# Kernel optimization log

Hardware: AMD Instinct MI355X
Metric: run time of the kernel (lower is better)

## Reference

```python
import jax, jax.numpy as jnp
import numpy as np

CPJ = 8
HID = 256
PARENTS = [-1,0,0,0,1,2,3,4,5,6,7,8,9,9,9,12,13,14,16,17,18,19]
SPARSE_IDX = list(range(54))

def _extend(nodes, cpj, parents=None):
    nodes = list(nodes)
    if parents is not None:
        while nodes[-1] != 0:
            nodes.append(parents[nodes[-1]])
    return [j * cpj + k for j in nodes for k in range(cpj)]

DQ_IN = _extend([0,3,6,9,12,13,14,15,16,17,18,19,20,21], CPJ, PARENTS)  # 21 nodes -> 168 ch
OUT1 = _extend([9], CPJ)          # 8 ch
OUT2 = _extend([6, 9, 12], CPJ)   # 24 ch
OUT3 = _extend([0, 3, 6], CPJ)    # 24 ch
IN_DIM = len(DQ_IN) + len(SPARSE_IDX)  # 222


def _mlp_params(key, out_dim):
    k = jax.random.split(key, 6)
    s = lambda fan_in: 1.0 / np.sqrt(fan_in)
    return (
        jax.random.uniform(k[0], (IN_DIM, HID), jnp.float32, -s(IN_DIM), s(IN_DIM)),
        jax.random.uniform(k[1], (HID,), jnp.float32, -s(IN_DIM), s(IN_DIM)),
        jax.random.uniform(k[2], (HID, HID), jnp.float32, -s(HID), s(HID)),
        jax.random.uniform(k[3], (HID,), jnp.float32, -s(HID), s(HID)),
        jax.random.uniform(k[4], (HID, out_dim), jnp.float32, -s(HID), s(HID)),
        jax.random.uniform(k[5], (out_dim,), jnp.float32, -s(HID), s(HID)),
    )


def setup_inputs() -> dict:
    key = jax.random.key(0)
    ks = jax.random.split(key, 5)
    B, T = 1024, 128
    inp = {
        'sparse_input': jax.random.normal(ks[0], (B, T, 54), jnp.float32),
        'decoder_output': jax.random.normal(ks[1], (B, T, 22 * CPJ), jnp.float32),
    }
    for i, (k, od) in enumerate(zip(ks[2:5], (len(OUT1), len(OUT2), len(OUT3))), start=1):
        p = _mlp_params(k, od)
        for j, name in enumerate(('w0', 'b0', 'w1', 'b1', 'w2', 'b2')):
            inp[f'{name}_{i}'] = p[j]
    return inp


def _mlp(x, w0, b0, w1, b1, w2, b2):
    h = jax.nn.leaky_relu(x @ w0 + b0, 0.01)
    h = jax.nn.leaky_relu(h @ w1 + b1, 0.01)
    return h @ w2 + b2


def reference(sparse_input, decoder_output,
              w0_1, b0_1, w1_1, b1_1, w2_1, b2_1,
              w0_2, b0_2, w1_2, b1_2, w2_2, b2_2,
              w0_3, b0_3, w1_3, b1_3, w2_3, b2_3):
    sp = sparse_input[:, :, jnp.array(SPARSE_IDX)]
    d = decoder_output
    # pass 1
    x = jnp.concatenate((d[:, :, jnp.array(DQ_IN)], sp), axis=2)
    res1 = _mlp(x, w0_1, b0_1, w1_1, b1_1, w2_1, b2_1)
    d = d.at[:, :, jnp.array(OUT1)].set(res1)
    # pass 2
    x = jnp.concatenate((d[:, :, jnp.array(DQ_IN)], sp), axis=2)
    res2 = _mlp(x, w0_2, b0_2, w1_2, b1_2, w2_2, b2_2)
    d = d.at[:, :, jnp.array(OUT2)].set(res2)
    # pass 3
    x = jnp.concatenate((d[:, :, jnp.array(DQ_IN)], sp), axis=2)
    res3 = _mlp(x, w0_3, b0_3, w1_3, b1_3, w2_3, b2_3)
    return res3
```

## Files before the change

kernel.cpp:

```cpp
#include <hip/hip_runtime.h>

typedef __bf16 bf16x8 __attribute__((ext_vector_type(8)));
typedef __bf16 bf16x4 __attribute__((ext_vector_type(4)));
typedef float  f32x16 __attribute__((ext_vector_type(16)));

#define DDEC  176
#define DSP   54
#define HID   256
#define RPW   32
#define WPB   4
#define BM    (RPW * WPB)
#define CSZ   8192
#define W1_OFF 65536
#define W2_OFF 131072
#define MLP_WS 139264

struct Biases { const float* b1[3]; const float* b2[3]; };

__global__ __launch_bounds__(256) void prep_weights(
    const float* __restrict__ w0a, const float* __restrict__ w1a, const float* __restrict__ w2a,
    const float* __restrict__ w0b, const float* __restrict__ w1b, const float* __restrict__ w2b,
    const float* __restrict__ w0c, const float* __restrict__ w1c, const float* __restrict__ w2c,
    const float* __restrict__ b0a, const float* __restrict__ b0b, const float* __restrict__ b0c,
    __bf16* __restrict__ ws)
{
  int idx = blockIdx.x * 256 + threadIdx.x;
  if (idx >= 3 * MLP_WS) return;
  int m = idx / MLP_WS;
  int r = idx - m * MLP_WS;
  const float* w0 = (m == 0) ? w0a : (m == 1) ? w0b : w0c;
  const float* w1 = (m == 0) ? w1a : (m == 1) ? w1b : w1c;
  const float* w2 = (m == 0) ? w2a : (m == 1) ? w2b : w2c;
  const float* b0 = (m == 0) ? b0a : (m == 1) ? b0b : b0c;
  float v;
  if (r < W1_OFF) {
    int n = r >> 8, k = r & 255;
    v = (k < 222) ? w0[k * HID + n] : (k == 222 ? b0[n] : 0.0f);
  } else if (r < W2_OFF) {
    int rr = r - W1_OFF;
    int n = rr >> 8, k = rr & 255;
    v = w1[k * HID + n];
  } else {
    int rr = r - W2_OFF;
    int n = rr >> 8, k = rr & 255;
    int od = (m == 0) ? 8 : 24;
    v = (n < od) ? w2[k * od + n] : 0.0f;
  }
  ws[idx] = (__bf16)v;
}

__device__ __forceinline__ float lrelu(float v) { return v > 0.f ? v : 0.01f * v; }

__device__ __forceinline__ void gload16(const void* g, void* l) {
  __builtin_amdgcn_global_load_lds(
      (const __attribute__((address_space(1))) void*)g,
      (__attribute__((address_space(3))) void*)l, 16, 0, 0);
}

__device__ __forceinline__ void stage(const __bf16* __restrict__ wsrc, __bf16* buf, int tid) {
  #pragma unroll
  for (int r = 0; r < 4; ++r) {
    const int a  = (r * 256 + tid) * 16;
    const int lc = a >> 9;
    const int un = (a & 511) ^ ((lc & 31) << 4);
    gload16(wsrc + lc * 256 + (un >> 1), (char*)buf + r * 4096 + (tid >> 6) * 1024);
  }
}

template<int NKK>
__device__ __forceinline__ void gemm1(const __bf16* buf, const bf16x8* bfr,
                                      f32x16& acc, int r32, int h) {
  const int sw = r32 << 4;
  const char* abase = (const char*)buf + (r32 << 9);
  #pragma unroll
  for (int kk = 0; kk < NKK; ++kk) {
    const int inner = ((kk << 5) + (h << 4)) ^ sw;
    bf16x8 a0 = *(const bf16x8*)(abase + inner);
    acc = __builtin_amdgcn_mfma_f32_32x32x16_bf16(a0, bfr[kk], acc, 0, 0, 0);
  }
}

__device__ __forceinline__ bf16x4 shfl32(bf16x4 x) {
  union { bf16x4 v; unsigned long long u; } t;
  t.v = x;
  t.u = __shfl_xor(t.u, 32, 64);
  return t.v;
}
__device__ __forceinline__ bf16x8 cat44(bf16x4 lo, bf16x4 hi) {
  return (bf16x8){lo[0], lo[1], lo[2], lo[3], hi[0], hi[1], hi[2], hi[3]};
}

struct Frag2 { bf16x8 f0, f1; };

template<bool BIAS, bool LR>
__device__ __forceinline__ Frag2 d2frags(const f32x16 acc, const float* bias, int h) {
  bf16x4 pk[4];
  #pragma unroll
  for (int t = 0; t < 4; ++t) {
    float bx = 0.f, by = 0.f, bz = 0.f, bw = 0.f;
    if (BIAS) {
      float4 bv = *(const float4*)(bias + 8 * t + 4 * h);
      bx = bv.x; by = bv.y; bz = bv.z; bw = bv.w;
    }
    float v0 = acc[4 * t] + bx, v1 = acc[4 * t + 1] + by;
    float v2 = acc[4 * t + 2] + bz, v3 = acc[4 * t + 3] + bw;
    if (LR) { v0 = lrelu(v0); v1 = lrelu(v1); v2 = lrelu(v2); v3 = lrelu(v3); }
    pk[t] = (bf16x4){(__bf16)v0, (__bf16)v1, (__bf16)v2, (__bf16)v3};
  }
  bf16x4 r1 = shfl32(h ? pk[0] : pk[1]);
  bf16x4 r2 = shfl32(h ? pk[2] : pk[3]);
  Frag2 out;
  out.f0 = h ? cat44(r1, pk[1]) : cat44(pk[0], r1);
  out.f1 = h ? cat44(r2, pk[3]) : cat44(pk[2], r2);
  return out;
}

__device__ __forceinline__ bf16x8 packf44(float4 a, float4 b) {
  return (bf16x8){(__bf16)a.x, (__bf16)a.y, (__bf16)a.z, (__bf16)a.w,
                  (__bf16)b.x, (__bf16)b.y, (__bf16)b.z, (__bf16)b.w};
}
__device__ __forceinline__ bf16x8 packf2222(float2 a, float2 b, float2 c, float2 d) {
  return (bf16x8){(__bf16)a.x, (__bf16)a.y, (__bf16)b.x, (__bf16)b.y,
                  (__bf16)c.x, (__bf16)c.y, (__bf16)d.x, (__bf16)d.y};
}

__global__ __launch_bounds__(256, 2) void trunk_fused(
    const float* __restrict__ sparse, const float* __restrict__ dec,
    const __bf16* __restrict__ ws, float* __restrict__ out, Biases bp)
{
  __shared__ __align__(16) __bf16 lds[16384];
  __bf16* const buf0 = lds;
  __bf16* const buf1 = lds + CSZ;

  const int tid  = threadIdx.x;
  const int lane = tid & 63;
  const int wid  = tid >> 6;
  const int r32  = lane & 31;
  const int h    = lane >> 5;
  const long grow = (long)blockIdx.x * BM + wid * RPW + r32;

  stage(ws, buf0, tid);

  bf16x8 xb[14];
  {
    constexpr int ND[21] = {0,3,6,9,12,13,14,15,16,17,18,19,20,21,19,17,14,9,6,3,0};
    const float* drow = dec + grow * DDEC;
    const float* srow = sparse + grow * DSP;
    #pragma unroll
    for (int kf = 0; kf < 14; ++kf) {
      if (kf <= 9) {
        const int off = (h ? ND[2 * kf + 1] : ND[2 * kf]) * 8;
        const float4* p = (const float4*)(drow + off);
        xb[kf] = packf44(p[0], p[1]);
      } else if (kf == 10) {
        if (h == 0) {
          const float4* p = (const float4*)(drow + ND[20] * 8);
          xb[kf] = packf44(p[0], p[1]);
        } else {
          const float2* q = (const float2*)(srow + 0);
          xb[kf] = packf2222(q[0], q[1], q[2], q[3]);
        }
      } else if (kf <= 12) {
        const float2* q = (const float2*)(srow + (2 * kf + h - 21) * 8);
        xb[kf] = packf2222(q[0], q[1], q[2], q[3]);
      } else {
        if (h == 0) {
          const float2* q = (const float2*)(srow + 40);
          xb[kf] = packf2222(q[0], q[1], q[2], q[3]);
        } else {
          const float2* q = (const float2*)(srow + 48);
          xb[kf] = packf2222(q[0], q[1], q[2], make_float2(1.0f, 0.0f));
        }
      }
    }
  }
  __syncthreads();
  int pb = 0;

  for (int m = 0; m < 3; ++m) {
    const __bf16* W0 = ws + m * MLP_WS;
    const __bf16* W1 = W0 + W1_OFF;
    const __bf16* W2 = W0 + W2_OFF;
    const float* b1 = bp.b1[m];
    const float* b2 = bp.b2[m];

    bf16x8 hb1[16];
    f32x16 a2 = {};

    #pragma unroll
    for (int c = 0; c < 8; ++c) {
      __bf16* cur = pb ? buf1 : buf0;
      __bf16* nxt = pb ? buf0 : buf1;
      stage(c < 7 ? W0 + (c + 1) * CSZ : W1, nxt, tid);
      f32x16 acc = {};
      gemm1<14>(cur, xb, acc, r32, h);
      Frag2 t = d2frags<false, true>(acc, nullptr, h);
      hb1[2 * c]     = t.f0;
      hb1[2 * c + 1] = t.f1;
      __syncthreads();
      pb ^= 1;
    }

    #pragma unroll
    for (int c = 0; c < 8; ++c) {
      __bf16* cur = pb ? buf1 : buf0;
      __bf16* nxt = pb ? buf0 : buf1;
      const __bf16* w2f = W2 + r32 * 256 + h * 8 + 32 * c;
      bf16x8 wa0 = *(const bf16x8*)(w2f + 0);
      bf16x8 wa1 = *(const bf16x8*)(w2f + 16);
      if (c < 7)      stage(W1 + (c + 1) * CSZ, nxt, tid);
      else if (m < 2) stage(ws + (m + 1) * MLP_WS, nxt, tid);
      f32x16 acc = {};
      gemm1<16>(cur, hb1, acc, r32, h);
      Frag2 t = d2frags<true, true>(acc, b1 + 32 * c, h);
      a2 = __builtin_amdgcn_mfma_f32_32x32x16_bf16(wa0, t.f0, a2, 0, 0, 0);
      a2 = __builtin_amdgcn_mfma_f32_32x32x16_bf16(wa1, t.f1, a2, 0, 0, 0);
      __syncthreads();
      pb ^= 1;
    }

    if (m == 2) {
      #pragma unroll
      for (int t = 0; t < 3; ++t) {
        const int c0 = 8 * t + 4 * h;
        float4 bv = *(const float4*)(b2 + c0);
        float4 o;
        o.x = a2[4 * t]     + bv.x;
        o.y = a2[4 * t + 1] + bv.y;
        o.z = a2[4 * t + 2] + bv.z;
        o.w = a2[4 * t + 3] + bv.w;
        *(float4*)(out + grow * 24 + c0) = o;
      }
    } else {
      bf16x4 pk[3];
      #pragma unroll
      for (int t = 0; t < 3; ++t) {
        const int c0 = 8 * t + 4 * h;
        float4 bv = *(const float4*)(b2 + c0);
        pk[t] = (bf16x4){(__bf16)(a2[4 * t] + bv.x),     (__bf16)(a2[4 * t + 1] + bv.y),
                         (__bf16)(a2[4 * t + 2] + bv.z), (__bf16)(a2[4 * t + 3] + bv.w)};
      }
      if (m == 0) {
        bf16x4 r = shfl32(pk[0]);
        if (h) { bf16x8 f = cat44(r, pk[0]); xb[1] = f; xb[8] = f; }
      } else {
        bf16x4 r1 = shfl32(h ? pk[0] : pk[1]);
        bf16x4 r2 = shfl32(pk[2]);
        if (h) {
          bf16x8 fJ9 = cat44(r1, pk[1]);  xb[1] = fJ9;  xb[8] = fJ9;
        } else {
          bf16x8 fJ6  = cat44(pk[0], r1); xb[1] = fJ6;  xb[9] = fJ6;
          bf16x8 fJ12 = cat44(pk[2], r2); xb[2] = fJ12;
        }
      }
    }
  }
}

extern "C" void kernel_launch(void* const* d_in, const int* in_sizes, int n_in,
                              void* d_out, int out_size, void* d_ws, size_t ws_size,
                              hipStream_t stream)
{
  const float* sparse = (const float*)d_in[0];
  const float* dec    = (const float*)d_in[1];
  Biases bp;
  const float* w0[3]; const float* w1[3]; const float* w2[3]; const float* b0[3];
  for (int m = 0; m < 3; ++m) {
    w0[m]    = (const float*)d_in[2 + m * 6 + 0];
    b0[m]    = (const float*)d_in[2 + m * 6 + 1];
    w1[m]    = (const float*)d_in[2 + m * 6 + 2];
    bp.b1[m] = (const float*)d_in[2 + m * 6 + 3];
    w2[m]    = (const float*)d_in[2 + m * 6 + 4];
    bp.b2[m] = (const float*)d_in[2 + m * 6 + 5];
  }
  __bf16* ws = (__bf16*)d_ws;
  const int nrows = in_sizes[0] / DSP;

  const int prep_total = 3 * MLP_WS;
  prep_weights<<<(prep_total + 255) / 256, 256, 0, stream>>>(
      w0[0], w1[0], w2[0], w0[1], w1[1], w2[1], w0[2], w1[2], w2[2],
      b0[0], b0[1], b0[2], ws);

  const int nblocks = nrows / BM;
  trunk_fused<<<nblocks, 256, 0, stream>>>(sparse, dec, ws, (float*)d_out, bp);
}
```

Baseline: 136.6 us.

## Stage weight chunks in pairs with split accumulators and LDS-cached biases

Doubles the weight staging chunk so each pipeline step covers 64 hidden columns. That halves the number of barrier and stage rounds per MLP and lets two independent MFMA chains run per k-step, and the first layer also splits accumulators by even and odd k to break the dependency chain. Biases are copied into LDS once, and s_setprio is raised around the MFMA sections. The cost is double the LDS per block (64KB for weights plus the bias area), which can cut occupancy below the 2-blocks-per-CU launch bound, and more accumulator registers.

```diff
diff --git a/kernel.cpp b/kernel.cpp
--- a/kernel.cpp
+++ b/kernel.cpp
@@ -11,6 +11,7 @@
 #define WPB   4
 #define BM    (RPW * WPB)
 #define CSZ   8192
+#define PSZ   16384
 #define W1_OFF 65536
 #define W2_OFF 131072
 #define MLP_WS 139264
@@ -57,9 +58,9 @@
       (__attribute__((address_space(3))) void*)l, 16, 0, 0);
 }
 
-__device__ __forceinline__ void stage(const __bf16* __restrict__ wsrc, __bf16* buf, int tid) {
+__device__ __forceinline__ void stage2(const __bf16* __restrict__ wsrc, __bf16* buf, int tid) {
   #pragma unroll
-  for (int r = 0; r < 4; ++r) {
+  for (int r = 0; r < 8; ++r) {
     const int a  = (r * 256 + tid) * 16;
     const int lc = a >> 9;
     const int un = (a & 511) ^ ((lc & 31) << 4);
@@ -68,15 +69,42 @@
 }
 
 template<int NKK>
-__device__ __forceinline__ void gemm1(const __bf16* buf, const bf16x8* bfr,
-                                      f32x16& acc, int r32, int h) {
+__device__ __forceinline__ void gemm_pair_split(const __bf16* bank, const bf16x8* bfr,
+                                                f32x16& oA, f32x16& oB, int r32, int h) {
   const int sw = r32 << 4;
-  const char* abase = (const char*)buf + (r32 << 9);
+  const char* c0 = (const char*)bank + (r32 << 9);
+  const char* c1 = c0 + 16384;
+  f32x16 a0 = {}, a1 = {}, b0 = {}, b1 = {};
   #pragma unroll
   for (int kk = 0; kk < NKK; ++kk) {
     const int inner = ((kk << 5) + (h << 4)) ^ sw;
-    bf16x8 a0 = *(const bf16x8*)(abase + inner);
-    acc = __builtin_amdgcn_mfma_f32_32x32x16_bf16(a0, bfr[kk], acc, 0, 0, 0);
+    bf16x8 fa = *(const bf16x8*)(c0 + inner);
+    bf16x8 fb = *(const bf16x8*)(c1 + inner);
+    if (kk & 1) {
+      a1 = __builtin_amdgcn_mfma_f32_32x32x16_bf16(fa, bfr[kk], a1, 0, 0, 0);
+      b1 = __builtin_amdgcn_mfma_f32_32x32x16_bf16(fb, bfr[kk], b1, 0, 0, 0);
+    } else {
+      a0 = __builtin_amdgcn_mfma_f32_32x32x16_bf16(fa, bfr[kk], a0, 0, 0, 0);
+      b0 = __builtin_amdgcn_mfma_f32_32x32x16_bf16(fb, bfr[kk], b0, 0, 0, 0);
+    }
+  }
+  oA = a0 + a1;
+  oB = b0 + b1;
+}
+
+template<int NKK>
+__device__ __forceinline__ void gemm_pair(const __bf16* bank, const bf16x8* bfr,
+                                          f32x16& accA, f32x16& accB, int r32, int h) {
+  const int sw = r32 << 4;
+  const char* c0 = (const char*)bank + (r32 << 9);
+  const char* c1 = c0 + 16384;
+  #pragma unroll
+  for (int kk = 0; kk < NKK; ++kk) {
+    const int inner = ((kk << 5) + (h << 4)) ^ sw;
+    bf16x8 fa = *(const bf16x8*)(c0 + inner);
+    bf16x8 fb = *(const bf16x8*)(c1 + inner);
+    accA = __builtin_amdgcn_mfma_f32_32x32x16_bf16(fa, bfr[kk], accA, 0, 0, 0);
+    accB = __builtin_amdgcn_mfma_f32_32x32x16_bf16(fb, bfr[kk], accB, 0, 0, 0);
   }
 }
 
@@ -128,9 +156,8 @@
     const float* __restrict__ sparse, const float* __restrict__ dec,
     const __bf16* __restrict__ ws, float* __restrict__ out, Biases bp)
 {
-  __shared__ __align__(16) __bf16 lds[16384];
-  __bf16* const buf0 = lds;
-  __bf16* const buf1 = lds + CSZ;
+  __shared__ __align__(16) __bf16 lds[2 * PSZ];
+  __shared__ __align__(16) float  bls[3 * 256 + 3 * 32];
 
   const int tid  = threadIdx.x;
   const int lane = tid & 63;
@@ -139,7 +166,19 @@
   const int h    = lane >> 5;
   const long grow = (long)blockIdx.x * BM + wid * RPW + r32;
 
-  stage(ws, buf0, tid);
+  stage2(ws, lds, tid);
+
+  {
+    #pragma unroll
+    for (int mm = 0; mm < 3; ++mm) bls[mm * 256 + tid] = bp.b1[mm][tid];
+    if (tid < 32) {
+      #pragma unroll
+      for (int mm = 0; mm < 3; ++mm) {
+        int od = (mm == 0) ? 8 : 24;
+        bls[768 + mm * 32 + tid] = (tid < od) ? bp.b2[mm][tid] : 0.f;
+      }
+    }
+  }
 
   bf16x8 xb[14];
   {
@@ -174,48 +213,61 @@
       }
     }
   }
-  __syncthreads();
   int pb = 0;
 
   for (int m = 0; m < 3; ++m) {
     const __bf16* W0 = ws + m * MLP_WS;
     const __bf16* W1 = W0 + W1_OFF;
     const __bf16* W2 = W0 + W2_OFF;
-    const float* b1 = bp.b1[m];
-    const float* b2 = bp.b2[m];
+    const float* b1l = bls + m * 256;
+    const float* b2l = bls + 768 + m * 32;
 
     bf16x8 hb1[16];
     f32x16 a2 = {};
 
     #pragma unroll
-    for (int c = 0; c < 8; ++c) {
-      __bf16* cur = pb ? buf1 : buf0;
-      __bf16* nxt = pb ? buf0 : buf1;
-      stage(c < 7 ? W0 + (c + 1) * CSZ : W1, nxt, tid);
-      f32x16 acc = {};
-      gemm1<14>(cur, xb, acc, r32, h);
-      Frag2 t = d2frags<false, true>(acc, nullptr, h);
-      hb1[2 * c]     = t.f0;
-      hb1[2 * c + 1] = t.f1;
+    for (int p = 0; p < 4; ++p) {
       __syncthreads();
+      __bf16* cur = lds + (pb ? PSZ : 0);
+      __bf16* nxt = lds + (pb ? 0 : PSZ);
+      stage2(p < 3 ? W0 + (p + 1) * PSZ : W1, nxt, tid);
+      f32x16 aA, aB;
+      __builtin_amdgcn_s_setprio(1);
+      gemm_pair_split<14>(cur, xb, aA, aB, r32, h);
+      __builtin_amdgcn_s_setprio(0);
+      Frag2 t0 = d2frags<false, true>(aA, nullptr, h);
+      Frag2 t1 = d2frags<false, true>(aB, nullptr, h);
+      hb1[4 * p]     = t0.f0;
+      hb1[4 * p + 1] = t0.f1;
+      hb1[4 * p + 2] = t1.f0;
+      hb1[4 * p + 3] = t1.f1;
       pb ^= 1;
     }
 
     #pragma unroll
-    for (int c = 0; c < 8; ++c) {
-      __bf16* cur = pb ? buf1 : buf0;
-      __bf16* nxt = pb ? buf0 : buf1;
-      const __bf16* w2f = W2 + r32 * 256 + h * 8 + 32 * c;
+    for (int p = 0; p < 4; ++p) {
+      __syncthreads();
+      __bf16* cur = lds + (pb ? PSZ : 0);
+      __bf16* nxt = lds + (pb ? 0 : PSZ);
+      const __bf16* w2f = W2 + r32 * 256 + h * 8 + 64 * p;
       bf16x8 wa0 = *(const bf16x8*)(w2f + 0);
       bf16x8 wa1 = *(const bf16x8*)(w2f + 16);
-      if (c < 7)      stage(W1 + (c + 1) * CSZ, nxt, tid);
-      else if (m < 2) stage(ws + (m + 1) * MLP_WS, nxt, tid);
-      f32x16 acc = {};
-      gemm1<16>(cur, hb1, acc, r32, h);
-      Frag2 t = d2frags<true, true>(acc, b1 + 32 * c, h);
-      a2 = __builtin_amdgcn_mfma_f32_32x32x16_bf16(wa0, t.f0, a2, 0, 0, 0);
-      a2 = __builtin_amdgcn_mfma_f32_32x32x16_bf16(wa1, t.f1, a2, 0, 0, 0);
-      __syncthreads();
+      bf16x8 wa2 = *(const bf16x8*)(w2f + 32);
+      bf16x8 wa3 = *(const bf16x8*)(w2f + 48);
+      if (p < 3)      stage2(W1 + (p + 1) * PSZ, nxt, tid);
+      else if (m < 2) stage2(ws + (m + 1) * MLP_WS, nxt, tid);
+      f32x16 accA = {}, accB = {};
+      __builtin_amdgcn_s_setprio(1);
+      gemm_pair<16>(cur, hb1, accA, accB, r32, h);
+      __builtin_amdgcn_s_setprio(0);
+      Frag2 tA = d2frags<true, true>(accA, b1l + 64 * p, h);
+      Frag2 tB = d2frags<true, true>(accB, b1l + 64 * p + 32, h);
+      __builtin_amdgcn_s_setprio(1);
+      a2 = __builtin_amdgcn_mfma_f32_32x32x16_bf16(wa0, tA.f0, a2, 0, 0, 0);
+      a2 = __builtin_amdgcn_mfma_f32_32x32x16_bf16(wa1, tA.f1, a2, 0, 0, 0);
+      a2 = __builtin_amdgcn_mfma_f32_32x32x16_bf16(wa2, tB.f0, a2, 0, 0, 0);
+      a2 = __builtin_amdgcn_mfma_f32_32x32x16_bf16(wa3, tB.f1, a2, 0, 0, 0);
+      __builtin_amdgcn_s_setprio(0);
       pb ^= 1;
     }
 
@@ -223,7 +275,7 @@
       #pragma unroll
       for (int t = 0; t < 3; ++t) {
         const int c0 = 8 * t + 4 * h;
-        float4 bv = *(const float4*)(b2 + c0);
+        float4 bv = *(const float4*)(b2l + c0);
         float4 o;
         o.x = a2[4 * t]     + bv.x;
         o.y = a2[4 * t + 1] + bv.y;
@@ -236,7 +288,7 @@
       #pragma unroll
       for (int t = 0; t < 3; ++t) {
         const int c0 = 8 * t + 4 * h;
-        float4 bv = *(const float4*)(b2 + c0);
+        float4 bv = *(const float4*)(b2l + c0);
         pk[t] = (bf16x4){(__bf16)(a2[4 * t] + bv.x),     (__bf16)(a2[4 * t + 1] + bv.y),
                          (__bf16)(a2[4 * t + 2] + bv.z), (__bf16)(a2[4 * t + 3] + bv.w)};
       }
```

Measured after the change: 137.3 us. Within noise of the previous version (+0.5%).

## Triple-buffer weight staging with single waitcnt-barrier and LDS-cached biases

Applied to the files above, without the earlier changes.

Replaces the double-buffered LDS weight pipeline with a three-slot ring that prefetches two chunks ahead. Each chunk now uses one s_waitcnt vmcnt(4) plus barrier instead of a trailing __syncthreads, so the next chunk's global-to-LDS loads can stay in flight during compute. Biases are copied into LDS once at kernel start instead of being read from global memory in the inner loop. The occupancy hint of 2 blocks per CU is dropped and LDS use grows, which may lower occupancy. The hand-written vmcnt count is fragile: other outstanding global loads, such as the W2 fragment reads, could make the wait insufficient.

```diff
diff --git a/kernel.cpp b/kernel.cpp
--- a/kernel.cpp
+++ b/kernel.cpp
@@ -67,6 +67,8 @@
   }
 }
 
+#define WAIT_BAR() asm volatile("s_waitcnt vmcnt(4)\n\ts_barrier" ::: "memory")
+
 template<int NKK>
 __device__ __forceinline__ void gemm1(const __bf16* buf, const bf16x8* bfr,
                                       f32x16& acc, int r32, int h) {
@@ -124,13 +126,12 @@
                   (__bf16)c.x, (__bf16)c.y, (__bf16)d.x, (__bf16)d.y};
 }
 
-__global__ __launch_bounds__(256, 2) void trunk_fused(
+__global__ __launch_bounds__(256) void trunk_fused(
     const float* __restrict__ sparse, const float* __restrict__ dec,
     const __bf16* __restrict__ ws, float* __restrict__ out, Biases bp)
 {
-  __shared__ __align__(16) __bf16 lds[16384];
-  __bf16* const buf0 = lds;
-  __bf16* const buf1 = lds + CSZ;
+  __shared__ __align__(16) __bf16 lds[3 * CSZ];
+  __shared__ __align__(16) float  bls[3 * 256 + 3 * 32];
 
   const int tid  = threadIdx.x;
   const int lane = tid & 63;
@@ -139,7 +140,20 @@
   const int h    = lane >> 5;
   const long grow = (long)blockIdx.x * BM + wid * RPW + r32;
 
-  stage(ws, buf0, tid);
+  stage(ws, lds, tid);
+  stage(ws + CSZ, lds + CSZ, tid);
+
+  {
+    #pragma unroll
+    for (int mm = 0; mm < 3; ++mm) bls[mm * 256 + tid] = bp.b1[mm][tid];
+    if (tid < 32) {
+      #pragma unroll
+      for (int mm = 0; mm < 3; ++mm) {
+        int od = (mm == 0) ? 8 : 24;
+        bls[768 + mm * 32 + tid] = (tid < od) ? bp.b2[mm][tid] : 0.f;
+      }
+    }
+  }
 
   bf16x8 xb[14];
   {
@@ -175,55 +189,59 @@
     }
   }
   __syncthreads();
-  int pb = 0;
+
+  __bf16 *P0 = lds, *P1 = lds + CSZ, *P2 = lds + 2 * CSZ;
 
   for (int m = 0; m < 3; ++m) {
     const __bf16* W0 = ws + m * MLP_WS;
     const __bf16* W1 = W0 + W1_OFF;
     const __bf16* W2 = W0 + W2_OFF;
-    const float* b1 = bp.b1[m];
-    const float* b2 = bp.b2[m];
+    const __bf16* W0n = ws + (m < 2 ? m + 1 : 2) * MLP_WS;
+    const float* b1l = bls + m * 256;
+    const float* b2l = bls + 768 + m * 32;
 
     bf16x8 hb1[16];
     f32x16 a2 = {};
 
     #pragma unroll
     for (int c = 0; c < 8; ++c) {
-      __bf16* cur = pb ? buf1 : buf0;
-      __bf16* nxt = pb ? buf0 : buf1;
-      stage(c < 7 ? W0 + (c + 1) * CSZ : W1, nxt, tid);
+      WAIT_BAR();
+      const __bf16* sp = (c <= 5) ? (W0 + (c + 2) * CSZ) : (W1 + (c - 6) * CSZ);
+      __bf16* tb = ((c + 2) % 3 == 0) ? P0 : ((c + 2) % 3 == 1) ? P1 : P2;
+      stage(sp, tb, tid);
+      const __bf16* cb = (c % 3 == 0) ? P0 : (c % 3 == 1) ? P1 : P2;
       f32x16 acc = {};
-      gemm1<14>(cur, xb, acc, r32, h);
+      gemm1<14>(cb, xb, acc, r32, h);
       Frag2 t = d2frags<false, true>(acc, nullptr, h);
       hb1[2 * c]     = t.f0;
       hb1[2 * c + 1] = t.f1;
-      __syncthreads();
-      pb ^= 1;
     }
 
     #pragma unroll
-    for (int c = 0; c < 8; ++c) {
-      __bf16* cur = pb ? buf1 : buf0;
-      __bf16* nxt = pb ? buf0 : buf1;
-      const __bf16* w2f = W2 + r32 * 256 + h * 8 + 32 * c;
+    for (int cc = 0; cc < 8; ++cc) {
+      const int c = cc + 8;
+      WAIT_BAR();
+      const __bf16* w2f = W2 + r32 * 256 + h * 8 + 32 * cc;
       bf16x8 wa0 = *(const bf16x8*)(w2f + 0);
       bf16x8 wa1 = *(const bf16x8*)(w2f + 16);
-      if (c < 7)      stage(W1 + (c + 1) * CSZ, nxt, tid);
-      else if (m < 2) stage(ws + (m + 1) * MLP_WS, nxt, tid);
+      const __bf16* sp = (c <= 13) ? (W1 + (c - 6) * CSZ) : (W0n + (c - 14) * CSZ);
+      __bf16* tb = ((c + 2) % 3 == 0) ? P0 : ((c + 2) % 3 == 1) ? P1 : P2;
+      stage(sp, tb, tid);
+      const __bf16* cb = (c % 3 == 0) ? P0 : (c % 3 == 1) ? P1 : P2;
       f32x16 acc = {};
-      gemm1<16>(cur, hb1, acc, r32, h);
-      Frag2 t = d2frags<true, true>(acc, b1 + 32 * c, h);
+      gemm1<16>(cb, hb1, acc, r32, h);
+      Frag2 t = d2frags<true, true>(acc, b1l + 32 * cc, h);
       a2 = __builtin_amdgcn_mfma_f32_32x32x16_bf16(wa0, t.f0, a2, 0, 0, 0);
       a2 = __builtin_amdgcn_mfma_f32_32x32x16_bf16(wa1, t.f1, a2, 0, 0, 0);
-      __syncthreads();
-      pb ^= 1;
-    }
+    }
+
+    __bf16* tmp = P0; P0 = P1; P1 = P2; P2 = tmp;
 
     if (m == 2) {
       #pragma unroll
       for (int t = 0; t < 3; ++t) {
         const int c0 = 8 * t + 4 * h;
-        float4 bv = *(const float4*)(b2 + c0);
+        float4 bv = *(const float4*)(b2l + c0);
         float4 o;
         o.x = a2[4 * t]     + bv.x;
         o.y = a2[4 * t + 1] + bv.y;
@@ -236,7 +254,7 @@
       #pragma unroll
       for (int t = 0; t < 3; ++t) {
         const int c0 = 8 * t + 4 * h;
-        float4 bv = *(const float4*)(b2 + c0);
+        float4 bv = *(const float4*)(b2l + c0);
         pk[t] = (bf16x4){(__bf16)(a2[4 * t] + bv.x),     (__bf16)(a2[4 * t + 1] + bv.y),
                          (__bf16)(a2[4 * t + 2] + bv.z), (__bf16)(a2[4 * t + 3] + bv.w)};
       }
```

Result: slower. 196.5 us (+43.9%).

## Process two 32-row tiles per wave to reuse each staged weight chunk

Applied to the files above, without the earlier changes.

Each wave now handles 64 rows as two 32-row tiles that share every LDS weight fragment read, issuing two MFMAs per A-load. Each block covers twice as many rows, so the grid halves and weight staging through LDS is amortized over more rows. The per-thread register state (activations, hidden fragments, accumulators) roughly doubles, so launch bounds drop to one block per SM, which lowers occupancy and latency hiding and may cause spills.

```diff
diff --git a/kernel.cpp b/kernel.cpp
--- a/kernel.cpp
+++ b/kernel.cpp
@@ -7,7 +7,7 @@
 #define DDEC  176
 #define DSP   54
 #define HID   256
-#define RPW   32
+#define RPW   64
 #define WPB   4
 #define BM    (RPW * WPB)
 #define CSZ   8192
@@ -68,15 +68,17 @@
 }
 
 template<int NKK>
-__device__ __forceinline__ void gemm1(const __bf16* buf, const bf16x8* bfr,
-                                      f32x16& acc, int r32, int h) {
+__device__ __forceinline__ void gemm_dual(const __bf16* buf,
+                                          const bf16x8* bfrA, const bf16x8* bfrB,
+                                          f32x16& accA, f32x16& accB, int r32, int h) {
   const int sw = r32 << 4;
   const char* abase = (const char*)buf + (r32 << 9);
   #pragma unroll
   for (int kk = 0; kk < NKK; ++kk) {
     const int inner = ((kk << 5) + (h << 4)) ^ sw;
     bf16x8 a0 = *(const bf16x8*)(abase + inner);
-    acc = __builtin_amdgcn_mfma_f32_32x32x16_bf16(a0, bfr[kk], acc, 0, 0, 0);
+    accA = __builtin_amdgcn_mfma_f32_32x32x16_bf16(a0, bfrA[kk], accA, 0, 0, 0);
+    accB = __builtin_amdgcn_mfma_f32_32x32x16_bf16(a0, bfrB[kk], accB, 0, 0, 0);
   }
 }
 
@@ -124,11 +126,61 @@
                   (__bf16)c.x, (__bf16)c.y, (__bf16)d.x, (__bf16)d.y};
 }
 
-__global__ __launch_bounds__(256, 2) void trunk_fused(
+__device__ __forceinline__ void gather_x(bf16x8* xb, const float* dec_, const float* sp_,
+                                         long grow, int h) {
+  constexpr int ND[21] = {0,3,6,9,12,13,14,15,16,17,18,19,20,21,19,17,14,9,6,3,0};
+  const float* drow = dec_ + grow * DDEC;
+  const float* srow = sp_ + grow * DSP;
+  #pragma unroll
+  for (int kf = 0; kf < 14; ++kf) {
+    if (kf <= 9) {
+      const int off = (h ? ND[2 * kf + 1] : ND[2 * kf]) * 8;
+      const float4* p = (const float4*)(drow + off);
+      xb[kf] = packf44(p[0], p[1]);
+    } else if (kf == 10) {
+      if (h == 0) {
+        const float4* p = (const float4*)(drow + ND[20] * 8);
+        xb[kf] = packf44(p[0], p[1]);
+      } else {
+        const float2* q = (const float2*)(srow + 0);
+        xb[kf] = packf2222(q[0], q[1], q[2], q[3]);
+      }
+    } else if (kf <= 12) {
+      const float2* q = (const float2*)(srow + (2 * kf + h - 21) * 8);
+      xb[kf] = packf2222(q[0], q[1], q[2], q[3]);
+    } else {
+      if (h == 0) {
+        const float2* q = (const float2*)(srow + 40);
+        xb[kf] = packf2222(q[0], q[1], q[2], q[3]);
+      } else {
+        const float2* q = (const float2*)(srow + 48);
+        xb[kf] = packf2222(q[0], q[1], q[2], make_float2(1.0f, 0.0f));
+      }
+    }
+  }
+}
+
+__device__ __forceinline__ void patch_x(bf16x8* xb, const bf16x4* pk, int m, int h) {
+  if (m == 0) {
+    bf16x4 r = shfl32(pk[0]);
+    if (h) { bf16x8 f = cat44(r, pk[0]); xb[1] = f; xb[8] = f; }
+  } else {
+    bf16x4 r1 = shfl32(h ? pk[0] : pk[1]);
+    bf16x4 r2 = shfl32(pk[2]);
+    if (h) {
+      bf16x8 fJ9 = cat44(r1, pk[1]);  xb[1] = fJ9;  xb[8] = fJ9;
+    } else {
+      bf16x8 fJ6  = cat44(pk[0], r1); xb[1] = fJ6;  xb[9] = fJ6;
+      bf16x8 fJ12 = cat44(pk[2], r2); xb[2] = fJ12;
+    }
+  }
+}
+
+__global__ __launch_bounds__(256, 1) void trunk_fused(
     const float* __restrict__ sparse, const float* __restrict__ dec,
     const __bf16* __restrict__ ws, float* __restrict__ out, Biases bp)
 {
-  __shared__ __align__(16) __bf16 lds[16384];
+  __shared__ __align__(16) __bf16 lds[2 * CSZ];
   __bf16* const buf0 = lds;
   __bf16* const buf1 = lds + CSZ;
 
@@ -137,43 +189,14 @@
   const int wid  = tid >> 6;
   const int r32  = lane & 31;
   const int h    = lane >> 5;
-  const long grow = (long)blockIdx.x * BM + wid * RPW + r32;
+  const long growA = (long)blockIdx.x * BM + wid * RPW + r32;
+  const long growB = growA + 32;
 
   stage(ws, buf0, tid);
 
-  bf16x8 xb[14];
-  {
-    constexpr int ND[21] = {0,3,6,9,12,13,14,15,16,17,18,19,20,21,19,17,14,9,6,3,0};
-    const float* drow = dec + grow * DDEC;
-    const float* srow = sparse + grow * DSP;
-    #pragma unroll
-    for (int kf = 0; kf < 14; ++kf) {
-      if (kf <= 9) {
-        const int off = (h ? ND[2 * kf + 1] : ND[2 * kf]) * 8;
-        const float4* p = (const float4*)(drow + off);
-        xb[kf] = packf44(p[0], p[1]);
-      } else if (kf == 10) {
-        if (h == 0) {
-          const float4* p = (const float4*)(drow + ND[20] * 8);
-          xb[kf] = packf44(p[0], p[1]);
-        } else {
-          const float2* q = (const float2*)(srow + 0);
-          xb[kf] = packf2222(q[0], q[1], q[2], q[3]);
-        }
-      } else if (kf <= 12) {
-        const float2* q = (const float2*)(srow + (2 * kf + h - 21) * 8);
-        xb[kf] = packf2222(q[0], q[1], q[2], q[3]);
-      } else {
-        if (h == 0) {
-          const float2* q = (const float2*)(srow + 40);
-          xb[kf] = packf2222(q[0], q[1], q[2], q[3]);
-        } else {
-          const float2* q = (const float2*)(srow + 48);
-          xb[kf] = packf2222(q[0], q[1], q[2], make_float2(1.0f, 0.0f));
-        }
-      }
-    }
-  }
+  bf16x8 xbA[14], xbB[14];
+  gather_x(xbA, dec, sparse, growA, h);
+  gather_x(xbB, dec, sparse, growB, h);
   __syncthreads();
   int pb = 0;
 
@@ -184,19 +207,20 @@
     const float* b1 = bp.b1[m];
     const float* b2 = bp.b2[m];
 
-    bf16x8 hb1[16];
-    f32x16 a2 = {};
+    bf16x8 hbA[16], hbB[16];
+    f32x16 a2A = {}, a2B = {};
 
     #pragma unroll
     for (int c = 0; c < 8; ++c) {
       __bf16* cur = pb ? buf1 : buf0;
       __bf16* nxt = pb ? buf0 : buf1;
       stage(c < 7 ? W0 + (c + 1) * CSZ : W1, nxt, tid);
-      f32x16 acc = {};
-      gemm1<14>(cur, xb, acc, r32, h);
-      Frag2 t = d2frags<false, true>(acc, nullptr, h);
-      hb1[2 * c]     = t.f0;
-      hb1[2 * c + 1] = t.f1;
+      f32x16 accA = {}, accB = {};
+      gemm_dual<14>(cur, xbA, xbB, accA, accB, r32, h);
+      Frag2 tA = d2frags<false, true>(accA, nullptr, h);
+      Frag2 tB = d2frags<false, true>(accB, nullptr, h);
+      hbA[2 * c] = tA.f0;  hbA[2 * c + 1] = tA.f1;
+      hbB[2 * c] = tB.f0;  hbB[2 * c + 1] = tB.f1;
       __syncthreads();
       pb ^= 1;
     }
@@ -210,11 +234,14 @@
       bf16x8 wa1 = *(const bf16x8*)(w2f + 16);
       if (c < 7)      stage(W1 + (c + 1) * CSZ, nxt, tid);
       else if (m < 2) stage(ws + (m + 1) * MLP_WS, nxt, tid);
-      f32x16 acc = {};
-      gemm1<16>(cur, hb1, acc, r32, h);
-      Frag2 t = d2frags<true, true>(acc, b1 + 32 * c, h);
-      a2 = __builtin_amdgcn_mfma_f32_32x32x16_bf16(wa0, t.f0, a2, 0, 0, 0);
-      a2 = __builtin_amdgcn_mfma_f32_32x32x16_bf16(wa1, t.f1, a2, 0, 0, 0);
+      f32x16 accA = {}, accB = {};
+      gemm_dual<16>(cur, hbA, hbB, accA, accB, r32, h);
+      Frag2 tA = d2frags<true, true>(accA, b1 + 32 * c, h);
+      Frag2 tB = d2frags<true, true>(accB, b1 + 32 * c, h);
+      a2A = __builtin_amdgcn_mfma_f32_32x32x16_bf16(wa0, tA.f0, a2A, 0, 0, 0);
+      a2A = __builtin_amdgcn_mfma_f32_32x32x16_bf16(wa1, tA.f1, a2A, 0, 0, 0);
+      a2B = __builtin_amdgcn_mfma_f32_32x32x16_bf16(wa0, tB.f0, a2B, 0, 0, 0);
+      a2B = __builtin_amdgcn_mfma_f32_32x32x16_bf16(wa1, tB.f1, a2B, 0, 0, 0);
       __syncthreads();
       pb ^= 1;
     }
@@ -224,35 +251,27 @@
       for (int t = 0; t < 3; ++t) {
         const int c0 = 8 * t + 4 * h;
         float4 bv = *(const float4*)(b2 + c0);
-        float4 o;
-        o.x = a2[4 * t]     + bv.x;
-        o.y = a2[4 * t + 1] + bv.y;
-        o.z = a2[4 * t + 2] + bv.z;
-        o.w = a2[4 * t + 3] + bv.w;
-        *(float4*)(out + grow * 24 + c0) = o;
+        float4 oA, oB;
+        oA.x = a2A[4 * t]     + bv.x;  oB.x = a2B[4 * t]     + bv.x;
+        oA.y = a2A[4 * t + 1] + bv.y;  oB.y = a2B[4 * t + 1] + bv.y;
+        oA.z = a2A[4 * t + 2] + bv.z;  oB.z = a2B[4 * t + 2] + bv.z;
+        oA.w = a2A[4 * t + 3] + bv.w;  oB.w = a2B[4 * t + 3] + bv.w;
+        *(float4*)(out + growA * 24 + c0) = oA;
+        *(float4*)(out + growB * 24 + c0) = oB;
       }
     } else {
-      bf16x4 pk[3];
+      bf16x4 pkA[3], pkB[3];
       #pragma unroll
       for (int t = 0; t < 3; ++t) {
         const int c0 = 8 * t + 4 * h;
         float4 bv = *(const float4*)(b2 + c0);
-        pk[t] = (bf16x4){(__bf16)(a2[4 * t] + bv.x),     (__bf16)(a2[4 * t + 1] + bv.y),
-                         (__bf16)(a2[4 * t + 2] + bv.z), (__bf16)(a2[4 * t + 3] + bv.w)};
+        pkA[t] = (bf16x4){(__bf16)(a2A[4 * t] + bv.x),     (__bf16)(a2A[4 * t + 1] + bv.y),
+                          (__bf16)(a2A[4 * t + 2] + bv.z), (__bf16)(a2A[4 * t + 3] + bv.w)};
+        pkB[t] = (bf16x4){(__bf16)(a2B[4 * t] + bv.x),     (__bf16)(a2B[4 * t + 1] + bv.y),
+                          (__bf16)(a2B[4 * t + 2] + bv.z), (__bf16)(a2B[4 * t + 3] + bv.w)};
       }
-      if (m == 0) {
-        bf16x4 r = shfl32(pk[0]);
-        if (h) { bf16x8 f = cat44(r, pk[0]); xb[1] = f; xb[8] = f; }
-      } else {
-        bf16x4 r1 = shfl32(h ? pk[0] : pk[1]);
-        bf16x4 r2 = shfl32(pk[2]);
-        if (h) {
-          bf16x8 fJ9 = cat44(r1, pk[1]);  xb[1] = fJ9;  xb[8] = fJ9;
-        } else {
-          bf16x8 fJ6  = cat44(pk[0], r1); xb[1] = fJ6;  xb[9] = fJ6;
-          bf16x8 fJ12 = cat44(pk[2], r2); xb[2] = fJ12;
-        }
-      }
+      patch_x(xbA, pkA, m, h);
+      patch_x(xbB, pkB, m, h);
     }
   }
 }
```

Result: slower. 179.8 us (+31.6%).
